# Optimization experiments

Hardware: AMD Instinct MI355X
Metric: run time of the kernel (lower is better)

## Reference

```python
import jax, jax.numpy as jnp
import numpy as np

NHEAD = 8
ROUTING_STEPS = 2
TEMP = 1.0
ROPE_THETA = 10000.0


def rmsnorm(x, w, eps=1e-6):
    return x * jax.lax.rsqrt(jnp.mean(x * x, axis=-1, keepdims=True) + eps) * w


def rope_cos_sin(seq_len, head_dim, theta):
    inv = 1.0 / (theta ** (jnp.arange(0, head_dim, 2, dtype=jnp.float32) / head_dim))
    freqs = jnp.outer(jnp.arange(seq_len, dtype=jnp.float32), inv)  # [S, hd/2]
    return jnp.cos(freqs), jnp.sin(freqs)


def apply_rope(x, cos, sin):
    # x: [B,H,S,hd]; cos/sin: [S, hd/2]
    x1, x2 = x[..., 0::2], x[..., 1::2]
    c, s = cos[None, None], sin[None, None]
    r1 = x1 * c - x2 * s
    r2 = x1 * s + x2 * c
    return jnp.stack([r1, r2], axis=-1).reshape(x.shape)


def cube_forward(x, wq, wk, wv, wo, w1, w2, g1, g2, cos, sin):
    # Per-sample gathered expert weights: wq.. [B,D,D], w1 [B,D,F], w2 [B,F,D]
    B, S, D = x.shape
    H = NHEAD
    hd = D // H
    xn = rmsnorm(x, g1[:, None, :])
    q = jnp.einsum('bsd,bde->bse', xn, wq).reshape(B, S, H, hd).transpose(0, 2, 1, 3)
    k = jnp.einsum('bsd,bde->bse', xn, wk).reshape(B, S, H, hd).transpose(0, 2, 1, 3)
    v = jnp.einsum('bsd,bde->bse', xn, wv).reshape(B, S, H, hd).transpose(0, 2, 1, 3)
    q = apply_rope(q, cos, sin)
    k = apply_rope(k, cos, sin)
    scores = jnp.einsum('bhqd,bhkd->bhqk', q, k) / jnp.sqrt(jnp.float32(hd))
    causal = jnp.tril(jnp.ones((S, S), dtype=bool))
    scores = jnp.where(causal, scores, jnp.float32(-1e30))
    att = jax.nn.softmax(scores, axis=-1)
    o = jnp.einsum('bhqk,bhkd->bhqd', att, v).transpose(0, 2, 1, 3).reshape(B, S, D)
    x = x + jnp.einsum('bsd,bde->bse', o, wo)
    hn = rmsnorm(x, g2[:, None, :])
    ff = jax.nn.silu(jnp.einsum('bsd,bdf->bsf', hn, w1))
    return x + jnp.einsum('bsf,bfd->bsd', ff, w2)


def reference(input_ids, start_cubes, emb, Wq, Wk, Wv, Wo, W1, W2, n1, n2, gate_w, final_norm_w, fc_out_w):
    B, S = input_ids.shape
    D = emb.shape[1]
    C = Wq.shape[0]
    x = emb[input_ids] * jnp.sqrt(jnp.float32(D))
    cos, sin = rope_cos_sin(S, D // NHEAD, ROPE_THETA)
    # deterministic ring graph: neighbors of cube i are (i+1)%C and (i+2)%C
    ar = jnp.arange(C)
    adj = jnp.zeros((C, C), dtype=bool).at[ar, (ar + 1) % C].set(True).at[ar, (ar + 2) % C].set(True)
    cur = start_cubes
    acc_probs = jnp.zeros(C + 1, dtype=jnp.float32)
    acc_lb = jnp.float32(0.0)
    for _ in range(ROUTING_STEPS):
        x = cube_forward(x, Wq[cur], Wk[cur], Wv[cur], Wo[cur], W1[cur], W2[cur], n1[cur], n2[cur], cos, sin)
        pooled = x.mean(axis=1)                        # [B, D]
        scores = pooled @ gate_w                       # [B, C+1]
        probs = jax.nn.softmax(scores / TEMP, axis=-1)
        acc_probs = acc_probs + probs.sum(axis=0)
        avg = probs.mean(axis=0)
        acc_lb = acc_lb + (C + 1) * jnp.sum(avg * avg)
        masked = jnp.where(adj[cur], scores[:, :C], jnp.float32(-1e30))
        cur = jnp.argmax(masked, axis=-1)
    logits = jnp.einsum('bsd,dv->bsv', rmsnorm(x, final_norm_w), fc_out_w)
    avg_probs = acc_probs / jnp.float32(ROUTING_STEPS * B)
    aux_variance_loss = jnp.var(avg_probs)
    aux_lb_loss = acc_lb / jnp.float32(ROUTING_STEPS)
    return logits, aux_variance_loss, aux_lb_loss


def setup_inputs() -> dict:
    key = jax.random.key(0)
    ks = jax.random.split(key, 16)
    V, D, F, C, B, S = 32000, 512, 2048, 4, 2, 256
    w = 0.02
    return {
        'input_ids': jax.random.randint(ks[0], (B, S), 0, V),
        'start_cubes': jax.random.randint(ks[1], (B,), 0, C),
        'emb': jax.random.normal(ks[2], (V, D), jnp.float32) * w,
        'Wq': jax.random.normal(ks[3], (C, D, D), jnp.float32) * w,
        'Wk': jax.random.normal(ks[4], (C, D, D), jnp.float32) * w,
        'Wv': jax.random.normal(ks[5], (C, D, D), jnp.float32) * w,
        'Wo': jax.random.normal(ks[6], (C, D, D), jnp.float32) * w,
        'W1': jax.random.normal(ks[7], (C, D, F), jnp.float32) * w,
        'W2': jax.random.normal(ks[8], (C, F, D), jnp.float32) * w,
        'n1': jnp.ones((C, D), jnp.float32),
        'n2': jnp.ones((C, D), jnp.float32),
        'gate_w': jax.random.normal(ks[9], (D, C + 1), jnp.float32) * w,
        'final_norm_w': jnp.ones((D,), jnp.float32),
        'fc_out_w': jax.random.normal(ks[10], (D, V), jnp.float32) * w,
    }
```

## Files before the change

### kernel.cpp

```cpp
#include <hip/hip_runtime.h>
#include <hip/hip_bf16.h>

#define BB 2
#define SS 256
#define DDIM 512
#define HH 8
#define HDIM 64
#define FDIM 2048
#define CC 4
#define VV 32000
#define NTOK (BB*SS)
#define PCHUNK 16

typedef __hip_bfloat16 bf16;
typedef __attribute__((ext_vector_type(8))) short short8;
typedef __attribute__((ext_vector_type(4))) short short4v;
typedef __attribute__((ext_vector_type(4))) float floatx4;

__device__ __forceinline__ int get_mode(const unsigned* __restrict__ probe) {
    return (probe[0] == 0x3F800000u) ? 0 : 1;
}
__device__ __forceinline__ float ldw(const void* __restrict__ p, long i, int mode) {
    if (mode == 0) return ((const float*)p)[i];
    return __bfloat162float(((const bf16*)p)[i]);
}
__device__ __forceinline__ void stf(void* __restrict__ p, long i, float v, int mode) {
    if (mode == 0) ((float*)p)[i] = v;
    else ((bf16*)p)[i] = __float2bfloat16(v);
}

__device__ __forceinline__ void gload16(const void* g, void* l) {
    __builtin_amdgcn_global_load_lds(
        (const __attribute__((address_space(1))) unsigned int*)g,
        (__attribute__((address_space(3))) unsigned int*)l, 16, 0, 0);
}

__global__ void init_kernel(const int* __restrict__ ids,
                            const int* __restrict__ start_cubes,
                            const void* __restrict__ emb,
                            float* __restrict__ x,
                            float* __restrict__ acc_probs,
                            float* __restrict__ acc_lb,
                            int* __restrict__ cur,
                            const unsigned* __restrict__ probe) {
    int mode = get_mode(probe);
    int gid = blockIdx.x * blockDim.x + threadIdx.x;
    if (gid < NTOK * DDIM) {
        int tok = gid / DDIM, d = gid % DDIM;
        x[gid] = ldw(emb, (long)ids[tok] * DDIM + d, mode) * 22.627416997969522f;
    }
    if (gid < CC + 1) acc_probs[gid] = 0.f;
    if (gid == CC + 1) *acc_lb = 0.f;
    if (gid < BB) cur[gid] = start_cubes[gid];
}

__global__ void rmsnorm_kernel(const float* __restrict__ in,
                               void* __restrict__ out, int obf,
                               const void* __restrict__ gamma,
                               const int* __restrict__ cur,
                               float* __restrict__ zbuf, int zn,
                               const unsigned* __restrict__ probe) {
    int mode = get_mode(probe);
    int tok = blockIdx.x;
    int b = tok / SS;
    long goff = cur ? (long)cur[b] * DDIM : 0;
    if (zbuf) {
        int gtid = blockIdx.x * blockDim.x + threadIdx.x;
        int gstride = gridDim.x * blockDim.x;
        for (int i = gtid; i < zn; i += gstride) zbuf[i] = 0.f;
    }
    __shared__ float red[256];
    int t = threadIdx.x;
    float x0 = in[(long)tok * DDIM + t];
    float x1 = in[(long)tok * DDIM + t + 256];
    red[t] = x0 * x0 + x1 * x1;
    __syncthreads();
    for (int s = 128; s > 0; s >>= 1) {
        if (t < s) red[t] += red[t + s];
        __syncthreads();
    }
    float scale = rsqrtf(red[0] / DDIM + 1e-6f);
    float v0 = x0 * scale * ldw(gamma, goff + t, mode);
    float v1 = x1 * scale * ldw(gamma, goff + t + 256, mode);
    if (obf) {
        ((bf16*)out)[(long)tok * DDIM + t]       = __float2bfloat16(v0);
        ((bf16*)out)[(long)tok * DDIM + t + 256] = __float2bfloat16(v1);
    } else {
        ((float*)out)[(long)tok * DDIM + t]       = v0;
        ((float*)out)[(long)tok * DDIM + t + 256] = v1;
    }
}

__global__ void silu_kernel(const float* __restrict__ in,
                            ushort* __restrict__ out, int n) {
    int i4 = (blockIdx.x * blockDim.x + threadIdx.x) * 4;
    if (i4 >= n) return;
    float4 v = *(const float4*)&in[i4];
    float a = v.x / (1.f + expf(-v.x));
    float b = v.y / (1.f + expf(-v.y));
    float c = v.z / (1.f + expf(-v.z));
    float d = v.w / (1.f + expf(-v.w));
    bf16 t0 = __float2bfloat16(a), t1 = __float2bfloat16(b);
    bf16 t2 = __float2bfloat16(c), t3 = __float2bfloat16(d);
    short4v o;
    o[0] = *(short*)&t0; o[1] = *(short*)&t1;
    o[2] = *(short*)&t2; o[3] = *(short*)&t3;
    *(short4v*)&out[i4] = o;
}

__global__ void transpose_kernel(const void* __restrict__ in, bf16* __restrict__ out,
                                 int K, int N, long ims, long oms,
                                 const unsigned* __restrict__ probe) {
    int mode = get_mode(probe);
    __shared__ float tile[32][33];
    int mat = blockIdx.z;
    int n0 = blockIdx.x * 32, k0 = blockIdx.y * 32;
    int tx = threadIdx.x, ty = threadIdx.y;
#pragma unroll
    for (int i = 0; i < 4; i++)
        tile[ty + i * 8][tx] = ldw(in, (long)mat * ims + (long)(k0 + ty + i * 8) * N + (n0 + tx), mode);
    __syncthreads();
#pragma unroll
    for (int i = 0; i < 4; i++)
        out[(long)mat * oms + (long)(n0 + ty + i * 8) * K + (k0 + tx)] =
            __float2bfloat16(tile[tx][ty + i * 8]);
}

template <int BN>
__global__ __launch_bounds__(BN * 2)
void gemm_mfma(const ushort* __restrict__ A,
               const ushort* __restrict__ WtB,
               const int* __restrict__ cur, long wcube, long wz,
               int K, int N,
               const float* __restrict__ res,
               void* __restrict__ out, long ozstride,
               int omode, int ACT, int nsplit, int swz,
               const unsigned* __restrict__ probe) {
    constexpr int BLK = BN * 2;
    constexpr int CA  = 512 / BLK;
    constexpr int CB  = (BN * 4) / BLK;
    int mode = get_mode(probe);
    __shared__ __align__(16) ushort sA[2][128 * 32];
    __shared__ __align__(16) ushort sB[2][BN * 32];
    int tid = threadIdx.x;
    int mi = blockIdx.y, ni = blockIdx.x;
    if (swz) {
        int nb = gridDim.x, mb = gridDim.y;
        int lin = blockIdx.x + blockIdx.y * nb;
        int nwg = nb * mb;
        int q = nwg >> 3, r = nwg & 7;
        int xcd = lin & 7, pos = lin >> 3;
        int nid = (xcd < r ? xcd * (q + 1) : r * (q + 1) + (xcd - r) * q) + pos;
        mi = nid % mb;
        ni = nid / mb;
    }
    int m0 = mi * 128;
    int n0 = ni * BN;
    int z  = blockIdx.z / nsplit;
    int ks = blockIdx.z % nsplit;
    int Kc = K / nsplit;
    int kbeg = ks * Kc;
    const ushort* Wt = WtB + (long)z * wz + (cur ? (long)cur[m0 / SS] * wcube : 0);
    floatx4 acc[4][4];
#pragma unroll
    for (int i = 0; i < 4; i++)
#pragma unroll
        for (int j = 0; j < 4; j++)
#pragma unroll
            for (int r = 0; r < 4; r++) acc[i][j][r] = 0.f;
    int w = tid >> 6, lane = tid & 63;
    int wm = (w & 1) * 64;
    int wn = (w >> 1) * 64;
    int lr = lane & 15, quad = lane >> 4;

    auto stage = [&](int buf, int k0) {
#pragma unroll
        for (int i = 0; i < CA; i++) {
            int g  = tid + i * BLK;
            int gs = g ^ ((g >> 3) & 7);
            gload16(&A[(long)(m0 + (gs >> 2)) * K + k0 + (gs & 3) * 8], &sA[buf][g * 8]);
        }
#pragma unroll
        for (int i = 0; i < CB; i++) {
            int g  = tid + i * BLK;
            int gs = g ^ ((g >> 3) & 7);
            gload16(&Wt[(long)(n0 + (gs >> 2)) * K + k0 + (gs & 3) * 8], &sB[buf][g * 8]);
        }
    };

    int nsteps = Kc >> 5;
    stage(0, kbeg);
    for (int j = 0; j < nsteps; ++j) {
        int cu = j & 1;
        if (j + 1 < nsteps) {
            stage(cu ^ 1, kbeg + ((j + 1) << 5));
            if constexpr (CA + CB == 4)
                asm volatile("s_waitcnt vmcnt(4)" ::: "memory");
            else
                asm volatile("s_waitcnt vmcnt(3)" ::: "memory");
        } else {
            asm volatile("s_waitcnt vmcnt(0)" ::: "memory");
        }
        __builtin_amdgcn_sched_barrier(0);
        __builtin_amdgcn_s_barrier();
        short8 af[4], bfr[4];
#pragma unroll
        for (int i = 0; i < 4; i++) {
            int oA = (wm + i * 16 + lr) * 4 + quad;
            int sa = oA ^ ((oA >> 3) & 7);
            af[i]  = *(const short8*)&sA[cu][sa * 8];
            int oB = (wn + i * 16 + lr) * 4 + quad;
            int sb = oB ^ ((oB >> 3) & 7);
            bfr[i] = *(const short8*)&sB[cu][sb * 8];
        }
#pragma unroll
        for (int mm = 0; mm < 4; mm++)
#pragma unroll
            for (int nn = 0; nn < 4; nn++)
                acc[mm][nn] = __builtin_amdgcn_mfma_f32_16x16x32_bf16(af[mm], bfr[nn], acc[mm][nn], 0, 0, 0);
        asm volatile("s_waitcnt lgkmcnt(0)" ::: "memory");
        __builtin_amdgcn_sched_barrier(0);
        __builtin_amdgcn_s_barrier();
    }
#pragma unroll
    for (int mm = 0; mm < 4; mm++)
#pragma unroll
        for (int nn = 0; nn < 4; nn++) {
            int col = n0 + wn + nn * 16 + lr;
#pragma unroll
            for (int r = 0; r < 4; r++) {
                int row = m0 + wm + mm * 16 + quad * 4 + r;
                float v = acc[mm][nn][r];
                long oi = (long)z * ozstride + (long)row * N + col;
                if (omode == 3) {
                    atomicAdd((float*)out + oi, v);
                } else {
                    if (ACT == 1) v = v / (1.f + expf(-v));
                    if (res) v += res[(long)row * N + col];
                    if (omode == 0)      ((float*)out)[oi] = v;
                    else if (omode == 1) ((bf16*)out)[oi] = __float2bfloat16(v);
                    else                 stf(out, oi, v, mode);
                }
            }
        }
}

__global__ void rope_kernel(float* __restrict__ q, float* __restrict__ k) {
    int gid = blockIdx.x * blockDim.x + threadIdx.x;
    if (gid >= NTOK * HH * (HDIM / 2)) return;
    int j = gid % (HDIM / 2);
    int rest = gid / (HDIM / 2);
    int h = rest % HH;
    int tok = rest / HH;
    int s = tok % SS;
    float inv = expf(-(float)j * (logf(10000.f) / 32.f));
    float ang = (float)s * inv;
    float c = cosf(ang), sn = sinf(ang);
    long base = (long)tok * DDIM + h * HDIM + 2 * j;
    float q1 = q[base], q2 = q[base + 1];
    q[base]     = q1 * c - q2 * sn;
    q[base + 1] = q1 * sn + q2 * c;
    float k1 = k[base], k2 = k[base + 1];
    k[base]     = k1 * c - k2 * sn;
    k[base + 1] = k1 * sn + k2 * c;
}

__global__ void attn_kernel(const float* __restrict__ q,
                            const float* __restrict__ k,
                            const float* __restrict__ v,
                            void* __restrict__ o, int obf) {
    int blk = blockIdx.x;
    int qr = blk % SS;
    int h = (blk / SS) % HH;
    int b = blk / (SS * HH);
    int t = threadIdx.x;
    __shared__ float sc[256];
    __shared__ float red[256];
    __shared__ __align__(16) float qs[HDIM];
    long qbase = ((long)(b * SS + qr)) * DDIM + h * HDIM;
    if (t < HDIM) qs[t] = q[qbase + t];
    __syncthreads();
    float s = -1e30f;
    if (t <= qr) {
        long kbase = ((long)(b * SS + t)) * DDIM + h * HDIM;
        const float4* k4 = (const float4*)&k[kbase];
        const float4* q4 = (const float4*)qs;
        float acc = 0.f;
#pragma unroll
        for (int i = 0; i < HDIM / 4; i++) {
            float4 a = q4[i], bv = k4[i];
            acc += a.x * bv.x + a.y * bv.y + a.z * bv.z + a.w * bv.w;
        }
        s = acc * 0.125f;
    }
    sc[t] = s;
    red[t] = s;
    __syncthreads();
    for (int st = 128; st > 0; st >>= 1) {
        if (t < st) red[t] = fmaxf(red[t], red[t + st]);
        __syncthreads();
    }
    float m = red[0];
    __syncthreads();
    float e = (t <= qr) ? expf(sc[t] - m) : 0.f;
    sc[t] = e;
    red[t] = e;
    __syncthreads();
    for (int st = 128; st > 0; st >>= 1) {
        if (t < st) red[t] += red[t + st];
        __syncthreads();
    }
    float invsum = 1.f / red[0];
    __syncthreads();
    int g = t >> 6, d = t & 63;
    float pacc = 0.f;
    for (int kk = g; kk <= qr; kk += 4)
        pacc += sc[kk] * v[((long)(b * SS + kk)) * DDIM + h * HDIM + d];
    red[t] = pacc;
    __syncthreads();
    if (t < HDIM) {
        float vv = (red[t] + red[t + 64] + red[t + 128] + red[t + 192]) * invsum;
        if (obf) ((bf16*)o)[qbase + t] = __float2bfloat16(vv);
        else     ((float*)o)[qbase + t] = vv;
    }
}

__global__ void pool_partial_kernel(const float* __restrict__ x,
                                    float* __restrict__ partial) {
    int blk = blockIdx.x;
    int b = blk / (SS / PCHUNK);
    int c = blk % (SS / PCHUNK);
    int t = threadIdx.x;
    float acc = 0.f;
    long base = ((long)b * SS + c * PCHUNK) * DDIM + t;
#pragma unroll
    for (int i = 0; i < PCHUNK; i++) acc += x[base + (long)i * DDIM];
    partial[(long)blk * DDIM + t] = acc;
}

__global__ void routing_kernel(const float* __restrict__ partial,
                               const void* __restrict__ gate_w,
                               float* __restrict__ acc_probs,
                               float* __restrict__ acc_lb,
                               int* __restrict__ cur,
                               int final_step,
                               void* __restrict__ d_out,
                               const unsigned* __restrict__ probe) {
    int mode = get_mode(probe);
    __shared__ float wred[8][BB * (CC + 1)];
    __shared__ float scores[BB][CC + 1];
    int t = threadIdx.x;
    float pm[BB];
#pragma unroll
    for (int b = 0; b < BB; b++) {
        float acc = 0.f;
#pragma unroll
        for (int c = 0; c < SS / PCHUNK; c++)
            acc += partial[((long)b * (SS / PCHUNK) + c) * DDIM + t];
        pm[b] = acc / (float)SS;
    }
    float part[BB][CC + 1];
#pragma unroll
    for (int c = 0; c <= CC; c++) {
        float g = ldw(gate_w, (long)t * (CC + 1) + c, mode);
#pragma unroll
        for (int b = 0; b < BB; b++) part[b][c] = pm[b] * g;
    }
#pragma unroll
    for (int off = 32; off > 0; off >>= 1)
#pragma unroll
        for (int b = 0; b < BB; b++)
#pragma unroll
            for (int c = 0; c <= CC; c++)
                part[b][c] += __shfl_down(part[b][c], off);
    int wave = t >> 6, lane = t & 63;
    if (lane == 0)
#pragma unroll
        for (int b = 0; b < BB; b++)
#pragma unroll
            for (int c = 0; c <= CC; c++)
                wred[wave][b * (CC + 1) + c] = part[b][c];
    __syncthreads();
    if (t == 0) {
        for (int b = 0; b < BB; b++)
            for (int c = 0; c <= CC; c++) {
                float s = 0.f;
                for (int wv = 0; wv < 8; wv++) s += wred[wv][b * (CC + 1) + c];
                scores[b][c] = s;
            }
        float probs[BB][CC + 1];
        for (int b = 0; b < BB; b++) {
            float m = -1e30f;
            for (int c = 0; c <= CC; c++) m = fmaxf(m, scores[b][c]);
            float sum = 0.f;
            for (int c = 0; c <= CC; c++) { probs[b][c] = expf(scores[b][c] - m); sum += probs[b][c]; }
            for (int c = 0; c <= CC; c++) probs[b][c] /= sum;
        }
        float lb = 0.f;
        for (int c = 0; c <= CC; c++) {
            float sumb = 0.f;
            for (int b = 0; b < BB; b++) sumb += probs[b][c];
            acc_probs[c] += sumb;
            float avg = sumb / (float)BB;
            lb += avg * avg;
        }
        *acc_lb += (float)(CC + 1) * lb;
        for (int b = 0; b < BB; b++) {
            int cu = cur[b];
            int a1 = (cu + 1) % CC, a2 = (cu + 2) % CC;
            float best = -1e38f; int bi = 0;
            for (int c = 0; c < CC; c++) {
                float vv = (c == a1 || c == a2) ? scores[b][c] : -1e30f;
                if (vv > best) { best = vv; bi = c; }
            }
            cur[b] = bi;
        }
        if (final_step) {
            float ap[CC + 1], mean = 0.f;
            for (int c = 0; c <= CC; c++) { ap[c] = acc_probs[c] / (2.f * BB); mean += ap[c]; }
            mean /= (float)(CC + 1);
            float var = 0.f;
            for (int c = 0; c <= CC; c++) { float d = ap[c] - mean; var += d * d; }
            var /= (float)(CC + 1);
            stf(d_out, (long)NTOK * VV + 0, var, mode);
            stf(d_out, (long)NTOK * VV + 1, (*acc_lb) / 2.f, mode);
        }
    }
}

template <int TM, int ACT, bool OUT_DYN>
__global__ void gemm_kernel(const float* __restrict__ A,
                            const void* __restrict__ Wbase,
                            const int* __restrict__ cur, long wstride,
                            int K, int N,
                            const float* __restrict__ res,
                            void* __restrict__ out,
                            const unsigned* __restrict__ probe) {
    int mode = get_mode(probe);
    extern __shared__ float sA[];
    int row0 = blockIdx.y * TM;
    long woff = cur ? (long)cur[row0 / SS] * wstride : 0;
    int t = threadIdx.x;
    for (int i = t; i < TM * K; i += 256)
        sA[i] = A[(long)(row0 + i / K) * K + (i % K)];
    __syncthreads();
    int n = blockIdx.x * 256 + t;
    float acc[TM];
#pragma unroll
    for (int r = 0; r < TM; r++) acc[r] = 0.f;
    for (int k = 0; k < K; k++) {
        float w = ldw(Wbase, woff + (long)k * N + n, mode);
#pragma unroll
        for (int r = 0; r < TM; r++) acc[r] += sA[r * K + k] * w;
    }
#pragma unroll
    for (int r = 0; r < TM; r++) {
        float v = acc[r];
        if (ACT == 1) v = v / (1.f + expf(-v));
        if (res) v += res[(long)(row0 + r) * N + n];
        long oi = (long)(row0 + r) * N + n;
        if constexpr (OUT_DYN) stf(out, oi, v, mode);
        else                   ((float*)out)[oi] = v;
    }
}

__global__ void routing_kernel_fb(const float* __restrict__ x,
                                  const void* __restrict__ gate_w,
                                  float* __restrict__ acc_probs,
                                  float* __restrict__ acc_lb,
                                  int* __restrict__ cur,
                                  int final_step,
                                  void* __restrict__ d_out,
                                  const unsigned* __restrict__ probe) {
    int mode = get_mode(probe);
    __shared__ float pooled[BB][DDIM];
    __shared__ float scores[BB][CC + 1];
    int t = threadIdx.x;
    for (int b = 0; b < BB; b++) {
        float acc = 0.f;
        for (int s = 0; s < SS; s++) acc += x[((long)(b * SS + s)) * DDIM + t];
        pooled[b][t] = acc / (float)SS;
    }
    __syncthreads();
    if (t < BB * (CC + 1)) {
        int b = t / (CC + 1), c = t % (CC + 1);
        float acc = 0.f;
        for (int d = 0; d < DDIM; d++)
            acc += pooled[b][d] * ldw(gate_w, (long)d * (CC + 1) + c, mode);
        scores[b][c] = acc;
    }
    __syncthreads();
    if (t == 0) {
        float probs[BB][CC + 1];
        for (int b = 0; b < BB; b++) {
            float m = -1e30f;
            for (int c = 0; c <= CC; c++) m = fmaxf(m, scores[b][c]);
            float sum = 0.f;
            for (int c = 0; c <= CC; c++) { probs[b][c] = expf(scores[b][c] - m); sum += probs[b][c]; }
            for (int c = 0; c <= CC; c++) probs[b][c] /= sum;
        }
        float lb = 0.f;
        for (int c = 0; c <= CC; c++) {
            float sumb = 0.f;
            for (int b = 0; b < BB; b++) sumb += probs[b][c];
            acc_probs[c] += sumb;
            float avg = sumb / (float)BB;
            lb += avg * avg;
        }
        *acc_lb += (float)(CC + 1) * lb;
        for (int b = 0; b < BB; b++) {
            int cu = cur[b];
            int a1 = (cu + 1) % CC, a2 = (cu + 2) % CC;
            float best = -1e38f; int bi = 0;
            for (int c = 0; c < CC; c++) {
                float vv = (c == a1 || c == a2) ? scores[b][c] : -1e30f;
                if (vv > best) { best = vv; bi = c; }
            }
            cur[b] = bi;
        }
        if (final_step) {
            float ap[CC + 1], mean = 0.f;
            for (int c = 0; c <= CC; c++) { ap[c] = acc_probs[c] / (2.f * BB); mean += ap[c]; }
            mean /= (float)(CC + 1);
            float var = 0.f;
            for (int c = 0; c <= CC; c++) { float d = ap[c] - mean; var += d * d; }
            var /= (float)(CC + 1);
            stf(d_out, (long)NTOK * VV + 0, var, mode);
            stf(d_out, (long)NTOK * VV + 1, (*acc_lb) / 2.f, mode);
        }
    }
}

extern "C" void kernel_launch(void* const* d_in, const int* in_sizes, int n_in,
                              void* d_out, int out_size, void* d_ws, size_t ws_size,
                              hipStream_t stream) {
    const int*  ids   = (const int*)d_in[0];
    const int*  start = (const int*)d_in[1];
    const void* emb   = d_in[2];
    const void* Wq    = d_in[3];
    const void* Wk    = d_in[4];
    const void* Wv    = d_in[5];
    const void* Wo    = d_in[6];
    const void* W1    = d_in[7];
    const void* W2    = d_in[8];
    const void* n1    = d_in[9];
    const void* n2    = d_in[10];
    const void* gate  = d_in[11];
    const void* fnorm = d_in[12];
    const void* fcw   = d_in[13];
    const unsigned* probe = (const unsigned*)d_in[9];

    char* base = (char*)d_ws;
    size_t off = 0;
    auto alloc = [&](size_t bytes) { size_t p = off; off = (off + bytes + 255) & ~(size_t)255; return p; };
    size_t x_o    = alloc((size_t)NTOK * DDIM * 4);
    size_t qkv_o  = alloc((size_t)3 * NTOK * DDIM * 4);
    size_t xn_o   = alloc((size_t)NTOK * DDIM * 2);
    size_t ob_o   = alloc((size_t)NTOK * DDIM * 2);
    size_t ff_o   = alloc((size_t)NTOK * FDIM * 2);
    size_t ffp_o  = alloc((size_t)NTOK * FDIM * 4);
    size_t acc_o  = alloc(256);
    size_t part_o = alloc((size_t)BB * (SS / PCHUNK) * DDIM * 4);
    size_t qkvT_o = alloc((size_t)3 * CC * DDIM * DDIM * 2);
    size_t WoT_o  = alloc((size_t)CC * DDIM * DDIM * 2);
    size_t W1T_o  = alloc((size_t)CC * DDIM * FDIM * 2);
    size_t W2T_o  = alloc((size_t)CC * FDIM * DDIM * 2);
    size_t fcwT_o = alloc((size_t)DDIM * VV * 2);
    bool big = ws_size >= off;

    if (big) {
        float* x    = (float*)(base + x_o);
        float* qkv  = (float*)(base + qkv_o);
        float* q = qkv, *k = qkv + NTOK * DDIM, *v = qkv + 2 * NTOK * DDIM;
        bf16*  xn   = (bf16*)(base + xn_o);
        bf16*  ob   = (bf16*)(base + ob_o);
        bf16*  ff   = (bf16*)(base + ff_o);
        float* ffp  = (float*)(base + ffp_o);
        float* acc_probs = (float*)(base + acc_o);
        float* acc_lb = acc_probs + 8;
        int*   cur = (int*)(acc_lb + 8);
        float* partial = (float*)(base + part_o);
        bf16* qkvT = (bf16*)(base + qkvT_o);
        bf16* WoT  = (bf16*)(base + WoT_o);
        bf16* W1T  = (bf16*)(base + W1T_o);
        bf16* W2T  = (bf16*)(base + W2T_o);
        bf16* fcwT = (bf16*)(base + fcwT_o);

        dim3 tb(32, 8);
        transpose_kernel<<<dim3(16, 16, CC), tb, 0, stream>>>(Wq, qkvT,                 DDIM, DDIM, (long)DDIM*DDIM, (long)DDIM*DDIM, probe);
        transpose_kernel<<<dim3(16, 16, CC), tb, 0, stream>>>(Wk, qkvT +   CC*DDIM*DDIM, DDIM, DDIM, (long)DDIM*DDIM, (long)DDIM*DDIM, probe);
        transpose_kernel<<<dim3(16, 16, CC), tb, 0, stream>>>(Wv, qkvT + 2*CC*DDIM*DDIM, DDIM, DDIM, (long)DDIM*DDIM, (long)DDIM*DDIM, probe);
        transpose_kernel<<<dim3(16, 16, CC), tb, 0, stream>>>(Wo, WoT,  DDIM, DDIM, (long)DDIM*DDIM, (long)DDIM*DDIM, probe);
        transpose_kernel<<<dim3(64, 16, CC), tb, 0, stream>>>(W1, W1T,  DDIM, FDIM, (long)DDIM*FDIM, (long)FDIM*DDIM, probe);
        transpose_kernel<<<dim3(16, 64, CC), tb, 0, stream>>>(W2, W2T,  FDIM, DDIM, (long)FDIM*DDIM, (long)DDIM*FDIM, probe);
        transpose_kernel<<<dim3(1000, 16, 1), tb, 0, stream>>>(fcw, fcwT, DDIM, VV, 0, 0, probe);

        init_kernel<<<(NTOK * DDIM + 255) / 256, 256, 0, stream>>>(
            ids, start, emb, x, acc_probs, acc_lb, cur, probe);

        const long DD2 = (long)DDIM * DDIM;
        const int QS = 4;
        const int OS = 4;
        const int F1S = 4;
        const int F2S = 8;
        for (int step = 0; step < 2; step++) {
            rmsnorm_kernel<<<NTOK, 256, 0, stream>>>(x, xn, 1, n1, cur,
                                                     qkv, 3 * NTOK * DDIM, probe);
            gemm_mfma<256><<<dim3(DDIM/256, NTOK/128, 3*QS), 512, 0, stream>>>(
                (const ushort*)xn, (const ushort*)qkvT, cur, DD2, (long)CC*DD2,
                DDIM, DDIM, nullptr, qkv, (long)NTOK*DDIM, 3, 0, QS, 0, probe);
            rope_kernel<<<(NTOK * HH * (HDIM / 2) + 255) / 256, 256, 0, stream>>>(q, k);
            attn_kernel<<<BB * HH * SS, 256, 0, stream>>>(q, k, v, ob, 1);
            gemm_mfma<256><<<dim3(DDIM/256, NTOK/128, OS), 512, 0, stream>>>(
                (const ushort*)ob, (const ushort*)WoT, cur, DD2, 0,
                DDIM, DDIM, nullptr, x, 0, 3, 0, OS, 0, probe);
            rmsnorm_kernel<<<NTOK, 256, 0, stream>>>(x, xn, 1, n2, cur,
                                                     ffp, NTOK * FDIM, probe);
            gemm_mfma<256><<<dim3(FDIM/256, NTOK/128, F1S), 512, 0, stream>>>(
                (const ushort*)xn, (const ushort*)W1T, cur, (long)FDIM*DDIM, 0,
                DDIM, FDIM, nullptr, ffp, 0, 3, 0, F1S, 0, probe);
            silu_kernel<<<(NTOK * FDIM / 4 + 255) / 256, 256, 0, stream>>>(
                ffp, (ushort*)ff, NTOK * FDIM);
            gemm_mfma<256><<<dim3(DDIM/256, NTOK/128, F2S), 512, 0, stream>>>(
                (const ushort*)ff, (const ushort*)W2T, cur, (long)DDIM*FDIM, 0,
                FDIM, DDIM, nullptr, x, 0, 3, 0, F2S, 0, probe);
            pool_partial_kernel<<<BB * (SS / PCHUNK), 512, 0, stream>>>(x, partial);
            routing_kernel<<<1, 512, 0, stream>>>(
                partial, gate, acc_probs, acc_lb, cur, step == 1, d_out, probe);
        }
        rmsnorm_kernel<<<NTOK, 256, 0, stream>>>(x, xn, 1, fnorm, nullptr,
                                                 nullptr, 0, probe);
        gemm_mfma<128><<<dim3(VV/128, NTOK/128, 1), 256, 0, stream>>>(
            (const ushort*)xn, (const ushort*)fcwT, nullptr, 0, 0,
            DDIM, VV, nullptr, d_out, 0, 2, 0, 1, 1, probe);
        return;
    }

    float* ws = (float*)d_ws;
    float* x  = ws;
    float* xn = x  + NTOK * DDIM;
    float* q  = xn + NTOK * DDIM;
    float* k  = q  + NTOK * DDIM;
    float* v  = k  + NTOK * DDIM;
    float* o  = v  + NTOK * DDIM;
    float* ff = o  + NTOK * DDIM;
    float* acc_probs = ff + NTOK * FDIM;
    float* acc_lb    = acc_probs + 8;
    int*   cur       = (int*)(acc_lb + 8);
    const long DD2 = (long)DDIM * DDIM;

    init_kernel<<<(NTOK * DDIM + 255) / 256, 256, 0, stream>>>(
        ids, start, emb, x, acc_probs, acc_lb, cur, probe);
    for (int step = 0; step < 2; step++) {
        rmsnorm_kernel<<<NTOK, 256, 0, stream>>>(x, xn, 0, n1, cur, nullptr, 0, probe);
        dim3 gdd(DDIM / 256, NTOK / 16);
        size_t smem16 = 16 * DDIM * sizeof(float);
        gemm_kernel<16, 0, false><<<gdd, 256, smem16, stream>>>(
            xn, Wq, cur, DD2, DDIM, DDIM, nullptr, q, probe);
        gemm_kernel<16, 0, false><<<gdd, 256, smem16, stream>>>(
            xn, Wk, cur, DD2, DDIM, DDIM, nullptr, k, probe);
        gemm_kernel<16, 0, false><<<gdd, 256, smem16, stream>>>(
            xn, Wv, cur, DD2, DDIM, DDIM, nullptr, v, probe);
        rope_kernel<<<(NTOK * HH * (HDIM / 2) + 255) / 256, 256, 0, stream>>>(q, k);
        attn_kernel<<<BB * HH * SS, 256, 0, stream>>>(q, k, v, o, 0);
        gemm_kernel<16, 0, false><<<gdd, 256, smem16, stream>>>(
            o, Wo, cur, DD2, DDIM, DDIM, x, x, probe);
        rmsnorm_kernel<<<NTOK, 256, 0, stream>>>(x, xn, 0, n2, cur, nullptr, 0, probe);
        dim3 gdf(FDIM / 256, NTOK / 16);
        gemm_kernel<16, 1, false><<<gdf, 256, smem16, stream>>>(
            xn, W1, cur, (long)DDIM * FDIM, DDIM, FDIM, nullptr, ff, probe);
        dim3 gfd(DDIM / 256, NTOK / 4);
        size_t smem4f = 4 * FDIM * sizeof(float);
        gemm_kernel<4, 0, false><<<gfd, 256, smem4f, stream>>>(
            ff, W2, cur, (long)FDIM * DDIM, FDIM, DDIM, x, x, probe);
        routing_kernel_fb<<<1, 512, 0, stream>>>(
            x, gate, acc_probs, acc_lb, cur, step == 1, d_out, probe);
    }
    rmsnorm_kernel<<<NTOK, 256, 0, stream>>>(x, xn, 0, fnorm, nullptr, nullptr, 0, probe);
    dim3 gv(VV / 256, NTOK / 16);
    size_t smem16 = 16 * DDIM * sizeof(float);
    gemm_kernel<16, 0, true><<<gv, 256, smem16, stream>>>(
        xn, fcw, nullptr, 0, DDIM, VV, nullptr, d_out, probe);
}
```

Before: 533.9 us.

## Double GEMM K-tile to 64 and fuse RoPE into attention via table

The MFMA GEMM now stages 64-wide K slices per pipeline step instead of 32, halving the number of barrier/wait iterations at the cost of double the LDS footprint. Separately, a precomputed cos/sin table replaces the standalone RoPE kernel, and RoPE is applied on the fly inside the attention kernel for q and k. This removes one kernel launch and a read-modify-write pass over q/k, but recomputes the k rotation for every query row.

```diff
diff --git a/kernel.cpp b/kernel.cpp
--- a/kernel.cpp
+++ b/kernel.cpp
@@ -52,6 +52,15 @@
     if (gid < CC + 1) acc_probs[gid] = 0.f;
     if (gid == CC + 1) *acc_lb = 0.f;
     if (gid < BB) cur[gid] = start_cubes[gid];
+}
+
+__global__ void rope_table_kernel(float2* __restrict__ rt) {
+    int gid = blockIdx.x * blockDim.x + threadIdx.x;
+    if (gid >= SS * 32) return;
+    int j = gid & 31, s = gid >> 5;
+    float inv = expf(-(float)j * (logf(10000.f) / 32.f));
+    float ang = (float)s * inv;
+    rt[gid] = make_float2(cosf(ang), sinf(ang));
 }
 
 __global__ void rmsnorm_kernel(const float* __restrict__ in,
@@ -137,11 +146,11 @@
                int omode, int ACT, int nsplit, int swz,
                const unsigned* __restrict__ probe) {
     constexpr int BLK = BN * 2;
-    constexpr int CA  = 512 / BLK;
-    constexpr int CB  = (BN * 4) / BLK;
+    constexpr int CA  = 1024 / BLK;
+    constexpr int CB  = (BN * 8) / BLK;
     int mode = get_mode(probe);
-    __shared__ __align__(16) ushort sA[2][128 * 32];
-    __shared__ __align__(16) ushort sB[2][BN * 32];
+    __shared__ __align__(16) ushort sA[2][128 * 64];
+    __shared__ __align__(16) ushort sB[2][BN * 64];
     int tid = threadIdx.x;
     int mi = blockIdx.y, ni = blockIdx.x;
     if (swz) {
@@ -178,46 +187,49 @@
         for (int i = 0; i < CA; i++) {
             int g  = tid + i * BLK;
             int gs = g ^ ((g >> 3) & 7);
-            gload16(&A[(long)(m0 + (gs >> 2)) * K + k0 + (gs & 3) * 8], &sA[buf][g * 8]);
+            gload16(&A[(long)(m0 + (gs >> 3)) * K + k0 + (gs & 7) * 8], &sA[buf][g * 8]);
         }
 #pragma unroll
         for (int i = 0; i < CB; i++) {
             int g  = tid + i * BLK;
             int gs = g ^ ((g >> 3) & 7);
-            gload16(&Wt[(long)(n0 + (gs >> 2)) * K + k0 + (gs & 3) * 8], &sB[buf][g * 8]);
+            gload16(&Wt[(long)(n0 + (gs >> 3)) * K + k0 + (gs & 7) * 8], &sB[buf][g * 8]);
         }
     };
 
-    int nsteps = Kc >> 5;
+    int nsteps = Kc >> 6;
     stage(0, kbeg);
     for (int j = 0; j < nsteps; ++j) {
         int cu = j & 1;
         if (j + 1 < nsteps) {
-            stage(cu ^ 1, kbeg + ((j + 1) << 5));
-            if constexpr (CA + CB == 4)
-                asm volatile("s_waitcnt vmcnt(4)" ::: "memory");
+            stage(cu ^ 1, kbeg + ((j + 1) << 6));
+            if constexpr (CA + CB == 8)
+                asm volatile("s_waitcnt vmcnt(8)" ::: "memory");
             else
-                asm volatile("s_waitcnt vmcnt(3)" ::: "memory");
+                asm volatile("s_waitcnt vmcnt(6)" ::: "memory");
         } else {
             asm volatile("s_waitcnt vmcnt(0)" ::: "memory");
         }
         __builtin_amdgcn_sched_barrier(0);
         __builtin_amdgcn_s_barrier();
-        short8 af[4], bfr[4];
-#pragma unroll
-        for (int i = 0; i < 4; i++) {
-            int oA = (wm + i * 16 + lr) * 4 + quad;
-            int sa = oA ^ ((oA >> 3) & 7);
-            af[i]  = *(const short8*)&sA[cu][sa * 8];
-            int oB = (wn + i * 16 + lr) * 4 + quad;
-            int sb = oB ^ ((oB >> 3) & 7);
-            bfr[i] = *(const short8*)&sB[cu][sb * 8];
-        }
-#pragma unroll
-        for (int mm = 0; mm < 4; mm++)
-#pragma unroll
-            for (int nn = 0; nn < 4; nn++)
-                acc[mm][nn] = __builtin_amdgcn_mfma_f32_16x16x32_bf16(af[mm], bfr[nn], acc[mm][nn], 0, 0, 0);
+#pragma unroll
+        for (int half = 0; half < 2; ++half) {
+            short8 af[4], bfr[4];
+#pragma unroll
+            for (int i = 0; i < 4; i++) {
+                int oA = (wm + i * 16 + lr) * 8 + quad + half * 4;
+                int sa = oA ^ ((oA >> 3) & 7);
+                af[i]  = *(const short8*)&sA[cu][sa * 8];
+                int oB = (wn + i * 16 + lr) * 8 + quad + half * 4;
+                int sb = oB ^ ((oB >> 3) & 7);
+                bfr[i] = *(const short8*)&sB[cu][sb * 8];
+            }
+#pragma unroll
+            for (int mm = 0; mm < 4; mm++)
+#pragma unroll
+                for (int nn = 0; nn < 4; nn++)
+                    acc[mm][nn] = __builtin_amdgcn_mfma_f32_16x16x32_bf16(af[mm], bfr[nn], acc[mm][nn], 0, 0, 0);
+        }
         asm volatile("s_waitcnt lgkmcnt(0)" ::: "memory");
         __builtin_amdgcn_sched_barrier(0);
         __builtin_amdgcn_s_barrier();
@@ -268,6 +280,7 @@
 __global__ void attn_kernel(const float* __restrict__ q,
                             const float* __restrict__ k,
                             const float* __restrict__ v,
+                            const float2* __restrict__ rt,
                             void* __restrict__ o, int obf) {
     int blk = blockIdx.x;
     int qr = blk % SS;
@@ -278,7 +291,16 @@
     __shared__ float red[256];
     __shared__ __align__(16) float qs[HDIM];
     long qbase = ((long)(b * SS + qr)) * DDIM + h * HDIM;
-    if (t < HDIM) qs[t] = q[qbase + t];
+    if (t < HDIM) {
+        if (rt) {
+            int j = t >> 1;
+            float2 cs = rt[qr * 32 + j];
+            float q1 = q[qbase + 2 * j], q2 = q[qbase + 2 * j + 1];
+            qs[t] = (t & 1) ? (q1 * cs.y + q2 * cs.x) : (q1 * cs.x - q2 * cs.y);
+        } else {
+            qs[t] = q[qbase + t];
+        }
+    }
     __syncthreads();
     float s = -1e30f;
     if (t <= qr) {
@@ -286,10 +308,23 @@
         const float4* k4 = (const float4*)&k[kbase];
         const float4* q4 = (const float4*)qs;
         float acc = 0.f;
-#pragma unroll
-        for (int i = 0; i < HDIM / 4; i++) {
-            float4 a = q4[i], bv = k4[i];
-            acc += a.x * bv.x + a.y * bv.y + a.z * bv.z + a.w * bv.w;
+        if (rt) {
+            const float4* rt4 = (const float4*)&rt[t * 32];
+#pragma unroll
+            for (int i = 0; i < HDIM / 4; i++) {
+                float4 kv = k4[i], cs2 = rt4[i], a = q4[i];
+                float r0 = kv.x * cs2.x - kv.y * cs2.y;
+                float r1 = kv.x * cs2.y + kv.y * cs2.x;
+                float r2 = kv.z * cs2.z - kv.w * cs2.w;
+                float r3 = kv.z * cs2.w + kv.w * cs2.z;
+                acc += a.x * r0 + a.y * r1 + a.z * r2 + a.w * r3;
+            }
+        } else {
+#pragma unroll
+            for (int i = 0; i < HDIM / 4; i++) {
+                float4 a = q4[i], bv = k4[i];
+                acc += a.x * bv.x + a.y * bv.y + a.z * bv.z + a.w * bv.w;
+            }
         }
         s = acc * 0.125f;
     }
@@ -561,6 +596,7 @@
     size_t ffp_o  = alloc((size_t)NTOK * FDIM * 4);
     size_t acc_o  = alloc(256);
     size_t part_o = alloc((size_t)BB * (SS / PCHUNK) * DDIM * 4);
+    size_t rt_o   = alloc((size_t)SS * 32 * 8);
     size_t qkvT_o = alloc((size_t)3 * CC * DDIM * DDIM * 2);
     size_t WoT_o  = alloc((size_t)CC * DDIM * DDIM * 2);
     size_t W1T_o  = alloc((size_t)CC * DDIM * FDIM * 2);
@@ -580,6 +616,7 @@
         float* acc_lb = acc_probs + 8;
         int*   cur = (int*)(acc_lb + 8);
         float* partial = (float*)(base + part_o);
+        float2* rt = (float2*)(base + rt_o);
         bf16* qkvT = (bf16*)(base + qkvT_o);
         bf16* WoT  = (bf16*)(base + WoT_o);
         bf16* W1T  = (bf16*)(base + W1T_o);
@@ -594,6 +631,7 @@
         transpose_kernel<<<dim3(64, 16, CC), tb, 0, stream>>>(W1, W1T,  DDIM, FDIM, (long)DDIM*FDIM, (long)FDIM*DDIM, probe);
         transpose_kernel<<<dim3(16, 64, CC), tb, 0, stream>>>(W2, W2T,  FDIM, DDIM, (long)FDIM*DDIM, (long)DDIM*FDIM, probe);
         transpose_kernel<<<dim3(1000, 16, 1), tb, 0, stream>>>(fcw, fcwT, DDIM, VV, 0, 0, probe);
+        rope_table_kernel<<<(SS * 32 + 255) / 256, 256, 0, stream>>>(rt);
 
         init_kernel<<<(NTOK * DDIM + 255) / 256, 256, 0, stream>>>(
             ids, start, emb, x, acc_probs, acc_lb, cur, probe);
@@ -609,8 +647,7 @@
             gemm_mfma<256><<<dim3(DDIM/256, NTOK/128, 3*QS), 512, 0, stream>>>(
                 (const ushort*)xn, (const ushort*)qkvT, cur, DD2, (long)CC*DD2,
                 DDIM, DDIM, nullptr, qkv, (long)NTOK*DDIM, 3, 0, QS, 0, probe);
-            rope_kernel<<<(NTOK * HH * (HDIM / 2) + 255) / 256, 256, 0, stream>>>(q, k);
-            attn_kernel<<<BB * HH * SS, 256, 0, stream>>>(q, k, v, ob, 1);
+            attn_kernel<<<BB * HH * SS, 256, 0, stream>>>(q, k, v, rt, ob, 1);
             gemm_mfma<256><<<dim3(DDIM/256, NTOK/128, OS), 512, 0, stream>>>(
                 (const ushort*)ob, (const ushort*)WoT, cur, DD2, 0,
                 DDIM, DDIM, nullptr, x, 0, 3, 0, OS, 0, probe);
@@ -662,7 +699,7 @@
         gemm_kernel<16, 0, false><<<gdd, 256, smem16, stream>>>(
             xn, Wv, cur, DD2, DDIM, DDIM, nullptr, v, probe);
         rope_kernel<<<(NTOK * HH * (HDIM / 2) + 255) / 256, 256, 0, stream>>>(q, k);
-        attn_kernel<<<BB * HH * SS, 256, 0, stream>>>(q, k, v, o, 0);
+        attn_kernel<<<BB * HH * SS, 256, 0, stream>>>(q, k, v, nullptr, o, 0);
         gemm_kernel<16, 0, false><<<gdd, 256, smem16, stream>>>(
             o, Wo, cur, DD2, DDIM, DDIM, x, x, probe);
         rmsnorm_kernel<<<NTOK, 256, 0, stream>>>(x, xn, 0, n2, cur, nullptr, 0, probe);
```

Result: slower. 551.6 us (+3.3%).
